# Kernel tuning notes

Hardware: AMD Instinct MI355X
Metric: run time of the kernel (lower is better)

The kernel has to match this reference:

```python
import jax, jax.numpy as jnp
import numpy as np

NEG_SLOPE = 0.2


def add_self_loops(edge_index, num_nodes):
    loop = jnp.arange(num_nodes, dtype=edge_index.dtype)
    loops = jnp.stack([loop, loop])  # [2, N]
    return jnp.concatenate([edge_index, loops], axis=1)


def gat_conv(x, edge_index, W, a_src, a_dst, b, concat=True):
    """PyG-style GATConv. a_src/a_dst: [1, H, C]. W: [F_in, H*C]."""
    N = x.shape[0]
    H, C = a_src.shape[1], a_src.shape[2]
    xp = (x @ W).reshape(N, H, C)                       # [N, H, C]
    alpha_src = (xp * a_src).sum(-1)                    # [N, H]
    alpha_dst = (xp * a_dst).sum(-1)                    # [N, H]
    src, dst = edge_index[0], edge_index[1]
    e = alpha_src[src] + alpha_dst[dst]                 # [E, H]
    e = jnp.where(e > 0, e, NEG_SLOPE * e)              # LeakyReLU(0.2)
    # per-destination segment softmax
    m = jax.ops.segment_max(e, dst, num_segments=N)     # [N, H]
    m = jnp.where(jnp.isfinite(m), m, 0.0)
    ez = jnp.exp(e - m[dst])
    s = jax.ops.segment_sum(ez, dst, num_segments=N)    # [N, H]
    alpha = ez / (s[dst] + 1e-16)                       # [E, H]
    msg = xp[src] * alpha[:, :, None]                   # [E, H, C]
    out = jax.ops.segment_sum(msg, dst, num_segments=N) # [N, H, C]
    out = out.reshape(N, H * C) if concat else out.mean(axis=1)
    return out + b


def setup_inputs() -> dict:
    key = jax.random.key(0)
    ks = jax.random.split(key, 16)
    N, F, E, CLS = 100000, 256, 1600000, 10
    x = jax.random.normal(ks[0], (N, F), dtype=jnp.float32)
    edge_index = jax.random.randint(ks[1], (2, E), 0, N, dtype=jnp.int64)

    def glorot(k, shape):
        fan = shape[0] + shape[-1] * (shape[1] if len(shape) == 3 else 1)
        return jax.random.uniform(k, shape, jnp.float32, -1.0, 1.0) * jnp.sqrt(6.0 / fan)

    return {
        "x": x, "edge_index": edge_index,
        "W1": glorot(ks[2], (F, 128)),  "a1s": glorot(ks[3], (1, 8, 16)),
        "a1d": glorot(ks[4], (1, 8, 16)), "b1": jnp.zeros((128,), jnp.float32),
        "W2": glorot(ks[5], (128, 64)), "a2s": glorot(ks[6], (1, 8, 8)),
        "a2d": glorot(ks[7], (1, 8, 8)),  "b2": jnp.zeros((64,), jnp.float32),
        "W3": glorot(ks[8], (64, CLS)), "a3s": glorot(ks[9], (1, 1, CLS)),
        "a3d": glorot(ks[10], (1, 1, CLS)), "b3": jnp.zeros((CLS,), jnp.float32),
    }


def reference(x, edge_index, W1, a1s, a1d, b1, W2, a2s, a2d, b2, W3, a3s, a3d, b3):
    ei = add_self_loops(edge_index, x.shape[0])
    h = jax.nn.elu(gat_conv(x, ei, W1, a1s, a1d, b1))
    h = jax.nn.elu(gat_conv(h, ei, W2, a2s, a2d, b2))
    h = gat_conv(h, ei, W3, a3s, a3d, b3)
    return jax.nn.log_softmax(h, axis=1)
```

## Files before the change

### kernel.cpp

```cpp
#include <hip/hip_runtime.h>
#include <hip/hip_bf16.h>
#include <math.h>


#define LEAKY(v) ((v) > 0.f ? (v) : 0.2f * (v))

typedef __bf16 bf16_t;
typedef __bf16 bf16x8 __attribute__((ext_vector_type(8)));
typedef __bf16 bf16x4 __attribute__((ext_vector_type(4)));
typedef float f32x4 __attribute__((ext_vector_type(4)));
typedef unsigned short u16x8 __attribute__((ext_vector_type(8)));

static __device__ __forceinline__ unsigned short bf_bits(float f) {
    bf16_t b = (bf16_t)f;
    return __builtin_bit_cast(unsigned short, b);
}
static __device__ __forceinline__ float bf_to_f(unsigned short u) {
    return __uint_as_float(((unsigned int)u) << 16);
}
static __device__ __forceinline__ float bperm_f(int byteaddr, float v) {
    return __uint_as_float((unsigned)__builtin_amdgcn_ds_bpermute(byteaddr, (int)__float_as_uint(v)));
}

constexpr int NB_MAX = 400;
constexpr int BCAP = 5120;

__global__ void zero_k(int* a, int n) {
    int i = blockIdx.x * blockDim.x + threadIdx.x;
    if (i < n) a[i] = 0;
}

__global__ __launch_bounds__(256) void partition_k(
        const int* __restrict__ src, const int* __restrict__ dst, int E, int NB,
        int* __restrict__ bcur, unsigned* __restrict__ staged) {
    __shared__ int hist[NB_MAX];
    __shared__ int bstart[NB_MAX + 1];
    __shared__ int cur[NB_MAX];
    __shared__ int gbase[NB_MAX];
    __shared__ unsigned words[4096];
    __shared__ unsigned short bidl[4096];
    int tid = threadIdx.x;
    int e0 = blockIdx.x * 4096;
    int cnt = E - e0; if (cnt > 4096) cnt = 4096;
    if (cnt <= 0) return;

    for (int b = tid; b < NB; b += 256) hist[b] = 0;
    __syncthreads();
    for (int i = tid; i < cnt; i += 256) atomicAdd(&hist[dst[e0 + i] >> 8], 1);
    __syncthreads();
    if (tid == 0) {
        int run = 0;
        for (int b = 0; b < NB; b++) { bstart[b] = run; run += hist[b]; }
        bstart[NB] = run;
    }
    __syncthreads();
    for (int b = tid; b < NB; b += 256) {
        cur[b] = bstart[b];
        gbase[b] = hist[b] ? atomicAdd(&bcur[b], hist[b]) : 0;
    }
    __syncthreads();
    for (int i = tid; i < cnt; i += 256) {
        int s = src[e0 + i], d = dst[e0 + i];
        int b = d >> 8;
        unsigned w = (unsigned)s | ((unsigned)(d & 255) << 17);
        int p = atomicAdd(&cur[b], 1);
        words[p] = w;
        bidl[p] = (unsigned short)b;
    }
    __syncthreads();
    for (int i = tid; i < cnt; i += 256) {
        int b = bidl[i];
        staged[(size_t)b * BCAP + gbase[b] + (i - bstart[b])] = words[i];
    }
}

__global__ void scan_nb_k(const int* __restrict__ bcur, int* __restrict__ ebase, int NB) {
    int lane = threadIdx.x;
    int CH = (NB + 63) / 64;
    int b0 = lane * CH;
    int v[8]; int s = 0;
#pragma unroll 8
    for (int k = 0; k < CH; k++) { int b = b0 + k; int t = (b < NB) ? bcur[b] : 0; if (k < 8) v[k] = t; s += t; }
    int orig = s;
    for (int off = 1; off < 64; off <<= 1) {
        int t = __shfl_up(s, off, 64);
        if (lane >= off) s += t;
    }
    int run = s - orig;
    for (int k = 0; k < CH; k++) { int b = b0 + k; if (b < NB) { ebase[b] = run; run += v[k]; } }
    if (lane == 63) ebase[NB] = run;
}

__global__ __launch_bounds__(256) void buildcsr_k(
        const unsigned* __restrict__ staged, const int* __restrict__ bcur,
        const int* __restrict__ ebase, int* __restrict__ offs, int* __restrict__ cols,
        int N, int NB) {
    __shared__ int h[256], hs[256], curl[256];
    __shared__ int colsl[BCAP];
    int b = blockIdx.x, tid = threadIdx.x;
    int n0 = b << 8;
    int ecnt = bcur[b];
    int base_g = ebase[b];
    const unsigned* sb = staged + (size_t)b * BCAP;

    h[tid] = 0;
    __syncthreads();
    for (int i = tid; i < ecnt; i += 256) atomicAdd(&h[sb[i] >> 17], 1);
    __syncthreads();
    int val = h[tid];
    hs[tid] = val; __syncthreads();
    for (int off = 1; off < 256; off <<= 1) {
        int t = (tid >= off) ? hs[tid - off] : 0;
        __syncthreads();
        hs[tid] += t;
        __syncthreads();
    }
    int excl = hs[tid] - val;
    curl[tid] = excl;
    if (n0 + tid < N) offs[n0 + tid] = base_g + excl;
    if (b == NB - 1 && tid == 0) offs[N] = base_g + ecnt;
    __syncthreads();
    for (int i = tid; i < ecnt; i += 256) {
        unsigned w = sb[i];
        int p = atomicAdd(&curl[w >> 17], 1);
        colsl[p] = (int)(w & 0x1FFFFu);
    }
    __syncthreads();
    for (int i = tid; i < ecnt; i += 256) cols[base_g + i] = colsl[i];
}

__global__ void prep_w_k(const float* __restrict__ W, short* __restrict__ Bfs,
                         int K, int N, int NT, int total) {
    int idx = blockIdx.x * blockDim.x + threadIdx.x;
    if (idx >= total) return;
    int lane = idx & 63;
    int t = idx >> 6;
    int ntile = t % NT, kstep = t / NT;
    int quad = lane >> 4, nl = lane & 15;
    int n = ntile * 16 + nl;
    bf16_t* dst = (bf16_t*)Bfs + (size_t)idx * 16;
#pragma unroll
    for (int j = 0; j < 8; j++) {
        int k = kstep * 32 + quad * 8 + j;
        float v = W[k * N + n];
        bf16_t h = (bf16_t)v;
        bf16_t l = (bf16_t)(v - (float)h);
        dst[j] = h;
        dst[8 + j] = l;
    }
}

template <int BM, int WMT, int WNT, int NWM, bool ABF16, int CHEAD, int K>
__global__ __launch_bounds__(256, 2) void mfma_gemm_k(
        const void* __restrict__ Av, const short* __restrict__ Bfs,
        unsigned short* __restrict__ Cb,
        const float* __restrict__ a_s, const float* __restrict__ a_d,
        float* __restrict__ out_as, float* __restrict__ out_ad,
        int M, int N, int NT) {
    constexpr int NWN = 4 / NWM;
    constexpr int BN = 16 * WNT * NWN;
    constexpr int KP = K + 8;
    __shared__ __align__(16) bf16_t As_hi[BM * KP];
    __shared__ __align__(16) bf16_t As_lo[ABF16 ? 16 : BM * KP];
    const bf16_t* Bf = (const bf16_t*)Bfs;

    int tid = threadIdx.x;
    int wave = tid >> 6, lane = tid & 63;
    int quad = lane >> 4, l16 = lane & 15;
    int wm = wave % NWM, wn = wave / NWM;
    int row0 = blockIdx.x * BM;
    int ntile0 = blockIdx.y * (BN / 16) + wn * WNT;

    if constexpr (!ABF16) {
        constexpr int CHUNKS = BM * K * 4 / (16 * 256);
        const float* A = (const float*)Av;
        f32x4 tmp[CHUNKS];
#pragma unroll
        for (int c = 0; c < CHUNKS; c++) {
            int ci = c * 256 + tid;
            int fi = ci * 4;
            int row = fi / K, k = fi % K;
            int grow = row0 + row;
            tmp[c] = (f32x4){0.f, 0.f, 0.f, 0.f};
            if (grow < M) tmp[c] = *(const f32x4*)(A + (size_t)grow * K + k);
        }
#pragma unroll
        for (int c = 0; c < CHUNKS; c++) {
            int ci = c * 256 + tid;
            int fi = ci * 4;
            int row = fi / K, k = fi % K;
            bf16x4 h, l;
#pragma unroll
            for (int j = 0; j < 4; j++) {
                bf16_t hh = (bf16_t)tmp[c][j];
                h[j] = hh;
                l[j] = (bf16_t)(tmp[c][j] - (float)hh);
            }
            *(bf16x4*)&As_hi[row * KP + k] = h;
            *(bf16x4*)&As_lo[row * KP + k] = l;
        }
    } else {
        constexpr int CHUNKS = BM * K * 2 / (16 * 256);
        const unsigned short* A = (const unsigned short*)Av;
        u16x8 tmp[CHUNKS];
#pragma unroll
        for (int c = 0; c < CHUNKS; c++) {
            int ci = c * 256 + tid;
            int ei = ci * 8;
            int row = ei / K, k = ei % K;
            int grow = row0 + row;
            tmp[c] = (u16x8){0, 0, 0, 0, 0, 0, 0, 0};
            if (grow < M) tmp[c] = *(const u16x8*)(A + (size_t)grow * K + k);
        }
#pragma unroll
        for (int c = 0; c < CHUNKS; c++) {
            int ci = c * 256 + tid;
            int ei = ci * 8;
            int row = ei / K, k = ei % K;
            *(u16x8*)&As_hi[row * KP + k] = tmp[c];
        }
    }
    __syncthreads();

    f32x4 acc[WMT][WNT];
#pragma unroll
    for (int i = 0; i < WMT; i++)
#pragma unroll
        for (int j = 0; j < WNT; j++) acc[i][j] = (f32x4){0.f, 0.f, 0.f, 0.f};

#pragma unroll
    for (int ks = 0; ks < K / 32; ks++) {
        bf16x8 ah[WMT], al[WMT];
#pragma unroll
        for (int i = 0; i < WMT; i++) {
            int rowl = wm * (WMT * 16) + i * 16 + l16;
            ah[i] = *(const bf16x8*)&As_hi[rowl * KP + ks * 32 + quad * 8];
            if (!ABF16) al[i] = *(const bf16x8*)&As_lo[rowl * KP + ks * 32 + quad * 8];
        }
        bf16x8 bh[WNT], bl[WNT];
#pragma unroll
        for (int j = 0; j < WNT; j++) {
            size_t base = ((size_t)(ks * NT + ntile0 + j) * 64 + lane) * 16;
            bh[j] = *(const bf16x8*)&Bf[base];
            bl[j] = *(const bf16x8*)&Bf[base + 8];
        }
#pragma unroll
        for (int i = 0; i < WMT; i++)
#pragma unroll
            for (int j = 0; j < WNT; j++) {
                acc[i][j] = __builtin_amdgcn_mfma_f32_16x16x32_bf16(ah[i], bh[j], acc[i][j], 0, 0, 0);
                if (!ABF16)
                    acc[i][j] = __builtin_amdgcn_mfma_f32_16x16x32_bf16(al[i], bh[j], acc[i][j], 0, 0, 0);
                acc[i][j] = __builtin_amdgcn_mfma_f32_16x16x32_bf16(ah[i], bl[j], acc[i][j], 0, 0, 0);
            }
    }

#pragma unroll
    for (int i = 0; i < WMT; i++) {
        int rbase = row0 + wm * (WMT * 16) + i * 16 + quad * 4;
#pragma unroll
        for (int j = 0; j < WNT; j++) {
            int gcol = (ntile0 + j) * 16 + l16;
#pragma unroll
            for (int r2 = 0; r2 < 4; r2++) {
                int grow = rbase + r2;
                if (grow < M) Cb[(size_t)grow * N + gcol] = bf_bits(acc[i][j][r2]);
            }
        }
    }

    const int Hh = N / CHEAD;
#pragma unroll
    for (int j = 0; j < WNT; j++) {
        int gcol = (ntile0 + j) * 16 + l16;
        float cs = a_s[gcol], cd = a_d[gcol];
#pragma unroll
        for (int i = 0; i < WMT; i++) {
            float ps[4], pd[4];
#pragma unroll
            for (int r2 = 0; r2 < 4; r2++) {
                ps[r2] = acc[i][j][r2] * cs;
                pd[r2] = acc[i][j][r2] * cd;
            }
#pragma unroll
            for (int off = 1; off < CHEAD; off <<= 1) {
#pragma unroll
                for (int r2 = 0; r2 < 4; r2++) {
                    ps[r2] += __shfl_xor(ps[r2], off, 64);
                    pd[r2] += __shfl_xor(pd[r2], off, 64);
                }
            }
            if ((l16 & (CHEAD - 1)) == 0) {
                int hd = gcol / CHEAD;
                int rb = row0 + wm * (WMT * 16) + i * 16 + quad * 4;
#pragma unroll
                for (int r2 = 0; r2 < 4; r2++) {
                    int grow = rb + r2;
                    if (grow < M) {
                        out_as[(size_t)grow * Hh + hd] = ps[r2];
                        out_ad[(size_t)grow * Hh + hd] = pd[r2];
                    }
                }
            }
        }
    }
}

template <int BM, int BN, int BK, int TM, int TN>
__global__ void gemm_k(const unsigned short* __restrict__ Ab, const float* __restrict__ B,
                       float* __restrict__ C, unsigned short* __restrict__ Cb,
                       int M, int Nc, int K) {
    __shared__ float As[BK][BM + 1];
    __shared__ float Bs[BK][BN + 1];
    int tx = threadIdx.x, ty = threadIdx.y;
    int tid = ty * blockDim.x + tx;
    const int nthreads = (BM / TM) * (BN / TN);
    int row0 = blockIdx.x * BM, col0 = blockIdx.y * BN;
    float acc[TM][TN];
#pragma unroll
    for (int i = 0; i < TM; i++)
#pragma unroll
        for (int j = 0; j < TN; j++) acc[i][j] = 0.f;

    for (int k0 = 0; k0 < K; k0 += BK) {
        for (int i = tid; i < BM * BK; i += nthreads) {
            int r = i / BK, kk = i % BK;
            int gr = row0 + r;
            As[kk][r] = (gr < M) ? bf_to_f(Ab[(size_t)gr * K + (k0 + kk)]) : 0.f;
        }
        for (int i = tid; i < BK * BN; i += nthreads) {
            int kk = i / BN, c = i % BN;
            int gc = col0 + c;
            Bs[kk][c] = (gc < Nc) ? B[(long)(k0 + kk) * Nc + gc] : 0.f;
        }
        __syncthreads();
#pragma unroll
        for (int kk = 0; kk < BK; ++kk) {
            float a[TM], b[TN];
#pragma unroll
            for (int i = 0; i < TM; i++) a[i] = As[kk][ty * TM + i];
#pragma unroll
            for (int j = 0; j < TN; j++) b[j] = Bs[kk][tx * TN + j];
#pragma unroll
            for (int i = 0; i < TM; i++)
#pragma unroll
                for (int j = 0; j < TN; j++) acc[i][j] = fmaf(a[i], b[j], acc[i][j]);
        }
        __syncthreads();
    }
#pragma unroll
    for (int i = 0; i < TM; i++) {
        int gr = row0 + ty * TM + i;
        if (gr >= M) continue;
#pragma unroll
        for (int j = 0; j < TN; j++) {
            int gc = col0 + tx * TN + j;
            if (gc < Nc) {
                C[(long)gr * Nc + gc] = acc[i][j];
                Cb[(long)gr * Nc + gc] = bf_bits(acc[i][j]);
            }
        }
    }
}

template <int H, int C>
__global__ void alpha_k(const float* __restrict__ xp, const float* __restrict__ a_s,
                        const float* __restrict__ a_d, float* __restrict__ out_s,
                        float* __restrict__ out_d, int NH) {
    int i = blockIdx.x * blockDim.x + threadIdx.x;
    if (i >= NH) return;
    int h = i % H;
    const float* v = xp + (long)i * C;
    float ss = 0.f, sd = 0.f;
#pragma unroll
    for (int c = 0; c < C; c++) {
        float x = v[c];
        ss = fmaf(x, a_s[h * C + c], ss);
        sd = fmaf(x, a_d[h * C + c], sd);
    }
    out_s[i] = ss;
    out_d[i] = sd;
}

template <bool DO_ELU>
__global__ void agg16_k(const unsigned short* __restrict__ xpb,
                        const float* __restrict__ asrc, const float* __restrict__ adst,
                        const int* __restrict__ offs, const int* __restrict__ cols,
                        const float* __restrict__ bias, unsigned short* __restrict__ outb,
                        int N) {
    int gtid = blockIdx.x * blockDim.x + threadIdx.x;
    int n = gtid >> 6;
    if (n >= N) return;
    int lane = threadIdx.x & 63;
    int j = lane >> 3, h = lane & 7;
    const int jb = j << 2;
    int start = offs[n], end = offs[n + 1];
    const unsigned* xp32 = (const unsigned*)xpb;

    unsigned uself = xp32[(size_t)n * 64 + lane];
    float ad_l = adst[n * 8 + h];
    float vs = asrc[n * 8 + h] + ad_l;
    vs = LEAKY(vs);

    float m_w = vs;
    float s = (j == 0) ? 1.f : 0.f;
    float m_f = bperm_f(jb, vs);
    float a0 = __uint_as_float(uself << 16);
    float a1 = __uint_as_float(uself & 0xffff0000u);

    for (int c0 = start; c0 < end; c0 += 16) {
        int e0 = c0 + j, e1 = c0 + 8 + j;
        bool ok0 = e0 < end, ok1 = e1 < end;
        int sl0 = ok0 ? cols[e0] : 0;
        int sl1 = ok1 ? cols[e1] : 0;
        unsigned u[16];
#pragma unroll
        for (int t = 0; t < 8; t++) {
            int srcj = __builtin_amdgcn_readlane(sl0, t * 8);
            u[t] = xp32[(size_t)srcj * 64 + lane];
        }
#pragma unroll
        for (int t = 0; t < 8; t++) {
            int srcj = __builtin_amdgcn_readlane(sl1, t * 8);
            u[8 + t] = xp32[(size_t)srcj * 64 + lane];
        }
        float v0 = -1e30f, v1 = -1e30f;
        if (ok0) { v0 = asrc[sl0 * 8 + h] + ad_l; v0 = LEAKY(v0); }
        if (ok1) { v1 = asrc[sl1 * 8 + h] + ad_l; v1 = LEAKY(v1); }
        float cm = fmaxf(v0, v1);
        cm = fmaxf(cm, __shfl_xor(cm, 8, 64));
        cm = fmaxf(cm, __shfl_xor(cm, 16, 64));
        cm = fmaxf(cm, __shfl_xor(cm, 32, 64));
        float mw_new = fmaxf(m_w, cm);
        float w0 = __expf(v0 - mw_new);
        float w1 = __expf(v1 - mw_new);
        s = s * __expf(m_w - mw_new) + w0 + w1;
        m_w = mw_new;
        float cmF = bperm_f(jb, cm);
        float mf_new = fmaxf(m_f, cmF);
        float scF = __expf(m_f - mf_new);
        m_f = mf_new;
        a0 *= scF; a1 *= scF;
        float wl[16];
#pragma unroll
        for (int t = 0; t < 8; t++) wl[t] = bperm_f(jb + t * 32, w0);
#pragma unroll
        for (int t = 0; t < 8; t++) wl[8 + t] = bperm_f(jb + t * 32, w1);
#pragma unroll
        for (int t = 0; t < 16; t++) {
            a0 = fmaf(wl[t], __uint_as_float(u[t] << 16), a0);
            a1 = fmaf(wl[t], __uint_as_float(u[t] & 0xffff0000u), a1);
        }
    }
    s += __shfl_xor(s, 8, 64);
    s += __shfl_xor(s, 16, 64);
    s += __shfl_xor(s, 32, 64);
    float rs = 1.f / (s + 1e-16f);
    float rsF = bperm_f(jb, rs);
    float o0 = a0 * rsF + bias[2 * lane];
    float o1 = a1 * rsF + bias[2 * lane + 1];
    if (DO_ELU) {
        o0 = o0 > 0.f ? o0 : __expf(o0) - 1.f;
        o1 = o1 > 0.f ? o1 : __expf(o1) - 1.f;
    }
    unsigned packed = (unsigned)bf_bits(o0) | ((unsigned)bf_bits(o1) << 16);
    ((unsigned*)outb)[(size_t)n * 64 + lane] = packed;
}

template <bool DO_ELU>
__global__ void agg8c8_k(const unsigned short* __restrict__ xpb,
                         const float* __restrict__ asrc, const float* __restrict__ adst,
                         const int* __restrict__ offs, const int* __restrict__ cols,
                         const float* __restrict__ bias, unsigned short* __restrict__ outb,
                         int N) {
    int gtid = blockIdx.x * blockDim.x + threadIdx.x;
    int n = gtid >> 6;
    if (n >= N) return;
    int lane = threadIdx.x & 63;
    int j = lane >> 3, h = lane & 7;
    int start = offs[n], end = offs[n + 1];
    const unsigned* xp32 = (const unsigned*)xpb;

    int fp = lane & 31;
    int hF = fp >> 2;
    int half = lane >> 5;
    int sbase = half * 32;

    float ad_l = adst[n * 8 + h];
    float vs = asrc[n * 8 + h] + ad_l;
    vs = LEAKY(vs);

    float m_w = vs;
    float s = (j == 0) ? 1.f : 0.f;
    float m_f = bperm_f(hF * 4, vs);
    float a0 = 0.f, a1 = 0.f;
    if (half == 0) {
        unsigned u = xp32[(size_t)n * 32 + fp];
        a0 = __uint_as_float(u << 16);
        a1 = __uint_as_float(u & 0xffff0000u);
    }

    for (int c0 = start; c0 < end; c0 += 16) {
        int e0 = c0 + j, e1 = c0 + 8 + j;
        bool ok0 = e0 < end, ok1 = e1 < end;
        int sl0 = ok0 ? cols[e0] : 0;
        int sl1 = ok1 ? cols[e1] : 0;
        int sv[8];
#pragma unroll
        for (int t = 0; t < 4; t++) sv[t] = __builtin_amdgcn_ds_bpermute(sbase + t * 64, sl0);
#pragma unroll
        for (int t = 0; t < 4; t++) sv[4 + t] = __builtin_amdgcn_ds_bpermute(sbase + t * 64, sl1);
        unsigned u[8];
#pragma unroll
        for (int t = 0; t < 8; t++) u[t] = xp32[(size_t)sv[t] * 32 + fp];
        float v0 = -1e30f, v1 = -1e30f;
        if (ok0) { v0 = asrc[sl0 * 8 + h] + ad_l; v0 = LEAKY(v0); }
        if (ok1) { v1 = asrc[sl1 * 8 + h] + ad_l; v1 = LEAKY(v1); }
        float cm = fmaxf(v0, v1);
        cm = fmaxf(cm, __shfl_xor(cm, 8, 64));
        cm = fmaxf(cm, __shfl_xor(cm, 16, 64));
        cm = fmaxf(cm, __shfl_xor(cm, 32, 64));
        float mw_new = fmaxf(m_w, cm);
        float w0 = __expf(v0 - mw_new);
        float w1 = __expf(v1 - mw_new);
        s = s * __expf(m_w - mw_new) + w0 + w1;
        m_w = mw_new;
        float cmF = bperm_f(hF * 4, cm);
        float mf_new = fmaxf(m_f, cmF);
        float scF = __expf(m_f - mf_new);
        m_f = mf_new;
        a0 *= scF; a1 *= scF;
        float wl[8];
#pragma unroll
        for (int t = 0; t < 4; t++) wl[t] = bperm_f(sbase + hF * 4 + t * 64, w0);
#pragma unroll
        for (int t = 0; t < 4; t++) wl[4 + t] = bperm_f(sbase + hF * 4 + t * 64, w1);
#pragma unroll
        for (int t = 0; t < 8; t++) {
            a0 = fmaf(wl[t], __uint_as_float(u[t] << 16), a0);
            a1 = fmaf(wl[t], __uint_as_float(u[t] & 0xffff0000u), a1);
        }
    }
    s += __shfl_xor(s, 8, 64);
    s += __shfl_xor(s, 16, 64);
    s += __shfl_xor(s, 32, 64);
    float rs = 1.f / (s + 1e-16f);
    float rsF = bperm_f(hF * 4, rs);
    a0 += __shfl_xor(a0, 32, 64);
    a1 += __shfl_xor(a1, 32, 64);
    if (half == 0) {
        float o0 = a0 * rsF + bias[2 * fp];
        float o1 = a1 * rsF + bias[2 * fp + 1];
        if (DO_ELU) {
            o0 = o0 > 0.f ? o0 : __expf(o0) - 1.f;
            o1 = o1 > 0.f ? o1 : __expf(o1) - 1.f;
        }
        unsigned packed = (unsigned)bf_bits(o0) | ((unsigned)bf_bits(o1) << 16);
        ((unsigned*)outb)[(size_t)n * 32 + fp] = packed;
    }
}

__global__ void agg1h_k(const unsigned short* __restrict__ xpb,
                        const float* __restrict__ asrc, const float* __restrict__ adst,
                        const int* __restrict__ offs, const int* __restrict__ cols,
                        const float* __restrict__ bias, float* __restrict__ out, int N) {
    int gtid = blockIdx.x * blockDim.x + threadIdx.x;
    int n = gtid >> 6;
    if (n >= N) return;
    int lane = threadIdx.x & 63;
    int start = offs[n], end = offs[n + 1];
    float ad = adst[n];
    float vs = asrc[n] + ad;
    vs = LEAKY(vs);

    float m, s;
    if (lane == 0) { m = vs; s = 1.f; } else { m = -1e30f; s = 0.f; }
    for (int e = start + lane; e < end; e += 64) {
        float v = asrc[cols[e]] + ad;
        v = LEAKY(v);
        float mo = fmaxf(m, v);
        s = s * __expf(m - mo) + __expf(v - mo);
        m = mo;
    }
#pragma unroll
    for (int off = 1; off <= 32; off <<= 1) {
        float mo = __shfl_xor(m, off, 64);
        float so = __shfl_xor(s, off, 64);
        float mn = fmaxf(m, mo);
        s = s * __expf(m - mn) + so * __expf(mo - mn);
        m = mn;
    }
    float rs = 1.f / (s + 1e-16f);
    float wself = __expf(vs - m) * rs;

    int j = lane / 10, c = lane - j * 10;
    float acc = 0.f;
    if (j == 0) acc = wself * bf_to_f(xpb[(size_t)n * 10 + c]);
    for (int c0 = start; c0 < end; c0 += 6) {
        int e = c0 + j;
        if (j < 6 && e < end) {
            int src = cols[e];
            float v = asrc[src] + ad;
            v = LEAKY(v);
            float w = __expf(v - m) * rs;
            acc = fmaf(w, bf_to_f(xpb[(size_t)src * 10 + c]), acc);
        }
    }
    float tot = acc;
#pragma unroll
    for (int k = 1; k < 6; k++) tot += __shfl(acc, lane + 10 * k, 64);

    float z = tot + bias[lane < 10 ? lane : 0];
    float mx = -1e30f;
#pragma unroll
    for (int k = 0; k < 10; k++) mx = fmaxf(mx, __shfl(z, k, 64));
    float se = 0.f;
#pragma unroll
    for (int k = 0; k < 10; k++) se += __expf(__shfl(z, k, 64) - mx);
    if (lane < 10) out[(size_t)n * 10 + lane] = z - (__logf(se) + mx);
}


static inline size_t alignup(size_t x) { return (x + 255) & ~(size_t)255; }

extern "C" void kernel_launch(void* const* d_in, const int* in_sizes, int n_in,
                              void* d_out, int out_size, void* d_ws, size_t ws_size,
                              hipStream_t stream) {
    const float* x   = (const float*)d_in[0];
    const int*   ei  = (const int*)d_in[1];
    const float* W1  = (const float*)d_in[2];
    const float* a1s = (const float*)d_in[3];
    const float* a1d = (const float*)d_in[4];
    const float* b1  = (const float*)d_in[5];
    const float* W2  = (const float*)d_in[6];
    const float* a2s = (const float*)d_in[7];
    const float* a2d = (const float*)d_in[8];
    const float* b2  = (const float*)d_in[9];
    const float* W3  = (const float*)d_in[10];
    const float* a3s = (const float*)d_in[11];
    const float* a3d = (const float*)d_in[12];
    const float* b3  = (const float*)d_in[13];
    float* out = (float*)d_out;

    const int N = in_sizes[0] / 256;
    const int E = in_sizes[1] / 2;
    const int* src = ei;
    const int* dst = ei + E;
    const int NB = (N + 255) >> 8;

    char* p = (char*)d_ws;
    int* offs    = (int*)p; p += alignup(sizeof(int) * (size_t)(N + 1));
    int* bcur    = (int*)p; p += alignup(sizeof(int) * (size_t)(NB_MAX + 1));
    int* ebase   = (int*)p; p += alignup(sizeof(int) * (size_t)(NB_MAX + 1));
    int* cols    = (int*)p; p += alignup(sizeof(int) * (size_t)E);
    unsigned short* xpb   = (unsigned short*)p; p += alignup(2 * (size_t)N * 128);
    unsigned short* hbufb = (unsigned short*)p; p += alignup(2 * (size_t)N * 128);
    float* xp    = (float*)p; p += alignup(sizeof(float) * (size_t)N * 128);
    float* as_   = (float*)p; p += alignup(sizeof(float) * (size_t)N * 8);
    float* ad_   = (float*)p; p += alignup(sizeof(float) * (size_t)N * 8);
    short* Bf1   = (short*)p; p += alignup(sizeof(short) * 8 * 8 * 64 * 16);
    short* Bf2   = (short*)p; p += alignup(sizeof(short) * 4 * 4 * 64 * 16);
    unsigned* staged = (unsigned*)xp;

    const int TB = 256;

    zero_k<<<(NB + TB - 1) / TB, TB, 0, stream>>>(bcur, NB);
    partition_k<<<(E + 4095) / 4096, 256, 0, stream>>>(src, dst, E, NB, bcur, staged);
    scan_nb_k<<<1, 64, 0, stream>>>(bcur, ebase, NB);
    buildcsr_k<<<NB, 256, 0, stream>>>(staged, bcur, ebase, offs, cols, N, NB);

    prep_w_k<<<(4096 + TB - 1) / TB, TB, 0, stream>>>(W1, Bf1, 256, 128, 8, 4096);
    prep_w_k<<<(1024 + TB - 1) / TB, TB, 0, stream>>>(W2, Bf2, 128, 64, 4, 1024);

    mfma_gemm_k<64, 4, 2, 1, false, 16, 256><<<dim3((N + 63) / 64, 1), 256, 0, stream>>>(
        x, Bf1, xpb, a1s, a1d, as_, ad_, N, 128, 8);
    agg16_k<true><<<(N * 64 + TB - 1) / TB, TB, 0, stream>>>(
        xpb, as_, ad_, offs, cols, b1, hbufb, N);

    mfma_gemm_k<64, 4, 1, 1, true, 8, 128><<<dim3((N + 63) / 64, 1), 256, 0, stream>>>(
        hbufb, Bf2, xpb, a2s, a2d, as_, ad_, N, 64, 4);
    agg8c8_k<true><<<(N * 64 + TB - 1) / TB, TB, 0, stream>>>(
        xpb, as_, ad_, offs, cols, b2, hbufb, N);

    gemm_k<64, 16, 16, 4, 1><<<dim3((N + 63) / 64, 1), dim3(16, 16), 0, stream>>>(
        hbufb, W3, xp, xpb, N, 10, 64);
    alpha_k<1, 10><<<(N + TB - 1) / TB, TB, 0, stream>>>(xp, a3s, a3d, as_, ad_, N);
    agg1h_k<<<(N * 64 + TB - 1) / TB, TB, 0, stream>>>(
        xpb, as_, ad_, offs, cols, b3, out, N);
}
```

Baseline: 526.3 us.

## Replace layer-3 scalar GEMM and alpha kernel with fused MFMA kernel

```diff
diff --git a/kernel.cpp b/kernel.cpp
--- a/kernel.cpp
+++ b/kernel.cpp
@@ -24,11 +24,6 @@
 
 constexpr int NB_MAX = 400;
 constexpr int BCAP = 5120;
-
-__global__ void zero_k(int* a, int n) {
-    int i = blockIdx.x * blockDim.x + threadIdx.x;
-    if (i < n) a[i] = 0;
-}
 
 __global__ __launch_bounds__(256) void partition_k(
         const int* __restrict__ src, const int* __restrict__ dst, int E, int NB,
@@ -150,6 +145,23 @@
     }
 }
 
+__global__ void prep_w3_k(const float* __restrict__ W, short* __restrict__ Bfs, int Nc) {
+    int idx = blockIdx.x * blockDim.x + threadIdx.x;
+    if (idx >= 128) return;
+    int lane = idx & 63, ks = idx >> 6;
+    int quad = lane >> 4, nl = lane & 15;
+    bf16_t* dst = (bf16_t*)Bfs + (size_t)idx * 16;
+#pragma unroll
+    for (int j = 0; j < 8; j++) {
+        int k = ks * 32 + quad * 8 + j;
+        float v = (nl < Nc) ? W[k * Nc + nl] : 0.f;
+        bf16_t h = (bf16_t)v;
+        bf16_t l = (bf16_t)(v - (float)h);
+        dst[j] = h;
+        dst[8 + j] = l;
+    }
+}
+
 template <int BM, int WMT, int WNT, int NWM, bool ABF16, int CHEAD, int K>
 __global__ __launch_bounds__(256, 2) void mfma_gemm_k(
         const void* __restrict__ Av, const short* __restrict__ Bfs,
@@ -306,80 +318,56 @@
     }
 }
 
-template <int BM, int BN, int BK, int TM, int TN>
-__global__ void gemm_k(const unsigned short* __restrict__ Ab, const float* __restrict__ B,
-                       float* __restrict__ C, unsigned short* __restrict__ Cb,
-                       int M, int Nc, int K) {
-    __shared__ float As[BK][BM + 1];
-    __shared__ float Bs[BK][BN + 1];
-    int tx = threadIdx.x, ty = threadIdx.y;
-    int tid = ty * blockDim.x + tx;
-    const int nthreads = (BM / TM) * (BN / TN);
-    int row0 = blockIdx.x * BM, col0 = blockIdx.y * BN;
-    float acc[TM][TN];
-#pragma unroll
-    for (int i = 0; i < TM; i++)
-#pragma unroll
-        for (int j = 0; j < TN; j++) acc[i][j] = 0.f;
-
-    for (int k0 = 0; k0 < K; k0 += BK) {
-        for (int i = tid; i < BM * BK; i += nthreads) {
-            int r = i / BK, kk = i % BK;
-            int gr = row0 + r;
-            As[kk][r] = (gr < M) ? bf_to_f(Ab[(size_t)gr * K + (k0 + kk)]) : 0.f;
-        }
-        for (int i = tid; i < BK * BN; i += nthreads) {
-            int kk = i / BN, c = i % BN;
-            int gc = col0 + c;
-            Bs[kk][c] = (gc < Nc) ? B[(long)(k0 + kk) * Nc + gc] : 0.f;
-        }
-        __syncthreads();
-#pragma unroll
-        for (int kk = 0; kk < BK; ++kk) {
-            float a[TM], b[TN];
-#pragma unroll
-            for (int i = 0; i < TM; i++) a[i] = As[kk][ty * TM + i];
-#pragma unroll
-            for (int j = 0; j < TN; j++) b[j] = Bs[kk][tx * TN + j];
-#pragma unroll
-            for (int i = 0; i < TM; i++)
-#pragma unroll
-                for (int j = 0; j < TN; j++) acc[i][j] = fmaf(a[i], b[j], acc[i][j]);
-        }
-        __syncthreads();
-    }
-#pragma unroll
-    for (int i = 0; i < TM; i++) {
-        int gr = row0 + ty * TM + i;
-        if (gr >= M) continue;
-#pragma unroll
-        for (int j = 0; j < TN; j++) {
-            int gc = col0 + tx * TN + j;
-            if (gc < Nc) {
-                C[(long)gr * Nc + gc] = acc[i][j];
-                Cb[(long)gr * Nc + gc] = bf_bits(acc[i][j]);
-            }
-        }
-    }
-}
-
-template <int H, int C>
-__global__ void alpha_k(const float* __restrict__ xp, const float* __restrict__ a_s,
-                        const float* __restrict__ a_d, float* __restrict__ out_s,
-                        float* __restrict__ out_d, int NH) {
-    int i = blockIdx.x * blockDim.x + threadIdx.x;
-    if (i >= NH) return;
-    int h = i % H;
-    const float* v = xp + (long)i * C;
-    float ss = 0.f, sd = 0.f;
-#pragma unroll
-    for (int c = 0; c < C; c++) {
-        float x = v[c];
-        ss = fmaf(x, a_s[h * C + c], ss);
-        sd = fmaf(x, a_d[h * C + c], sd);
-    }
-    out_s[i] = ss;
-    out_d[i] = sd;
+__global__ __launch_bounds__(256) void gemm3_k(
+        const unsigned short* __restrict__ Ab, const short* __restrict__ Bfs,
+        unsigned short* __restrict__ Cb,
+        const float* __restrict__ a_s, const float* __restrict__ a_d,
+        float* __restrict__ out_as, float* __restrict__ out_ad, int M) {
+    const bf16_t* Bf = (const bf16_t*)Bfs;
+    int tid = threadIdx.x;
+    int wave = tid >> 6, lane = tid & 63;
+    int quad = lane >> 4, l16 = lane & 15;
+    int grow0 = blockIdx.x * 64 + wave * 16;
+
+    bf16x8 bh[2], bl[2];
+#pragma unroll
+    for (int ks = 0; ks < 2; ks++) {
+        size_t base = (size_t)(ks * 64 + lane) * 16;
+        bh[ks] = *(const bf16x8*)&Bf[base];
+        bl[ks] = *(const bf16x8*)&Bf[base + 8];
+    }
+
+    int arow = grow0 + l16; if (arow >= M) arow = M - 1;
+    f32x4 acc = (f32x4){0.f, 0.f, 0.f, 0.f};
+#pragma unroll
+    for (int ks = 0; ks < 2; ks++) {
+        bf16x8 a = *(const bf16x8*)(Ab + (size_t)arow * 64 + ks * 32 + quad * 8);
+        acc = __builtin_amdgcn_mfma_f32_16x16x32_bf16(a, bh[ks], acc, 0, 0, 0);
+        acc = __builtin_amdgcn_mfma_f32_16x16x32_bf16(a, bl[ks], acc, 0, 0, 0);
+    }
+
+    bool colv = l16 < 10;
+    float cs = colv ? a_s[l16] : 0.f;
+    float cd = colv ? a_d[l16] : 0.f;
+    float ps[4], pd[4];
+#pragma unroll
+    for (int r = 0; r < 4; r++) { ps[r] = acc[r] * cs; pd[r] = acc[r] * cd; }
+#pragma unroll
+    for (int off = 1; off < 16; off <<= 1) {
+#pragma unroll
+        for (int r = 0; r < 4; r++) {
+            ps[r] += __shfl_xor(ps[r], off, 64);
+            pd[r] += __shfl_xor(pd[r], off, 64);
+        }
+    }
+#pragma unroll
+    for (int r = 0; r < 4; r++) {
+        int grow = grow0 + quad * 4 + r;
+        if (grow < M) {
+            if (colv) Cb[(size_t)grow * 10 + l16] = bf_bits(acc[r]);
+            if (l16 == 0) { out_as[grow] = ps[r]; out_ad[grow] = pd[r]; }
+        }
+    }
 }
 
 template <bool DO_ELU>
@@ -660,17 +648,19 @@
     float* ad_   = (float*)p; p += alignup(sizeof(float) * (size_t)N * 8);
     short* Bf1   = (short*)p; p += alignup(sizeof(short) * 8 * 8 * 64 * 16);
     short* Bf2   = (short*)p; p += alignup(sizeof(short) * 4 * 4 * 64 * 16);
+    short* Bf3   = (short*)p; p += alignup(sizeof(short) * 2 * 1 * 64 * 16);
     unsigned* staged = (unsigned*)xp;
 
     const int TB = 256;
 
-    zero_k<<<(NB + TB - 1) / TB, TB, 0, stream>>>(bcur, NB);
+    hipMemsetAsync(bcur, 0, sizeof(int) * (size_t)(NB + 1), stream);
     partition_k<<<(E + 4095) / 4096, 256, 0, stream>>>(src, dst, E, NB, bcur, staged);
     scan_nb_k<<<1, 64, 0, stream>>>(bcur, ebase, NB);
     buildcsr_k<<<NB, 256, 0, stream>>>(staged, bcur, ebase, offs, cols, N, NB);
 
     prep_w_k<<<(4096 + TB - 1) / TB, TB, 0, stream>>>(W1, Bf1, 256, 128, 8, 4096);
     prep_w_k<<<(1024 + TB - 1) / TB, TB, 0, stream>>>(W2, Bf2, 128, 64, 4, 1024);
+    prep_w3_k<<<1, 128, 0, stream>>>(W3, Bf3, 10);
 
     mfma_gemm_k<64, 4, 2, 1, false, 16, 256><<<dim3((N + 63) / 64, 1), 256, 0, stream>>>(
         x, Bf1, xpb, a1s, a1d, as_, ad_, N, 128, 8);
@@ -682,9 +672,8 @@
     agg8c8_k<true><<<(N * 64 + TB - 1) / TB, TB, 0, stream>>>(
         xpb, as_, ad_, offs, cols, b2, hbufb, N);
 
-    gemm_k<64, 16, 16, 4, 1><<<dim3((N + 63) / 64, 1), dim3(16, 16), 0, stream>>>(
-        hbufb, W3, xp, xpb, N, 10, 64);
-    alpha_k<1, 10><<<(N + TB - 1) / TB, TB, 0, stream>>>(xp, a3s, a3d, as_, ad_, N);
+    gemm3_k<<<(N + 63) / 64, 256, 0, stream>>>(
+        hbufb, Bf3, xpb, a3s, a3d, as_, ad_, N);
     agg1h_k<<<(N * 64 + TB - 1) / TB, TB, 0, stream>>>(
         xpb, as_, ad_, offs, cols, b3, out, N);
 }
```

Result: faster. 509.6 us (-3.2%).
